# Kernel tuning notes

Hardware: AMD Instinct MI355X
Metric: run time of the kernel (lower is better)

Reference implementation:

```python
import jax, jax.numpy as jnp
import numpy as np

B, DIN, DOUT, GRID_SIZE, SPLINE_ORDER, N_LAYERS = 4096, 1024, 1024, 8, 3, 2
COEFFS = GRID_SIZE + SPLINE_ORDER  # 11


def _kaiming_uniform(key, shape, fan_in):
    # torch nn.init.kaiming_uniform_ default: a=0 -> gain=sqrt(2), bound=sqrt(3)*gain/sqrt(fan_in)
    bound = float(np.sqrt(6.0 / fan_in))
    return jax.random.uniform(key, shape, jnp.float32, -bound, bound)


def setup_inputs() -> dict:
    key = jax.random.key(0)
    ks = jax.random.split(key, 1 + 3 * N_LAYERS)
    x = jax.random.normal(ks[0], (B, DIN), dtype=jnp.float32)
    # knot grid: arange(-so, gs+so+1)*h + lo, h=(hi-lo)/gs  -> shape [GRID_SIZE+2*SPLINE_ORDER+1]
    h = 2.0 / GRID_SIZE
    grid = jnp.arange(-SPLINE_ORDER, GRID_SIZE + SPLINE_ORDER + 1, dtype=jnp.float32) * h - 1.0
    base_w, spline_w, scaler = [], [], []
    for i in range(N_LAYERS):
        base_w.append(_kaiming_uniform(ks[1 + 3 * i], (DOUT, DIN), DIN))
        spline_w.append(_kaiming_uniform(ks[2 + 3 * i], (DOUT, DIN, COEFFS), DIN * COEFFS))
        scaler.append(_kaiming_uniform(ks[3 + 3 * i], (DOUT, DIN), DIN))
    return {
        "x": x,
        "base_w": jnp.stack(base_w),      # [L, DOUT, DIN]
        "spline_w": jnp.stack(spline_w),  # [L, DOUT, DIN, COEFFS]
        "scaler": jnp.stack(scaler),      # [L, DOUT, DIN]
        "grid": grid,                      # [G]
        "spline_order": SPLINE_ORDER,
    }


def b_splines(x, grid, spline_order):
    # x: (B, DIN) -> bases: (B, DIN, COEFFS) via Cox-de Boor recursion
    x = x[..., None]  # (B, DIN, 1)
    bases = ((x >= grid[:-1]) & (x < grid[1:])).astype(x.dtype)  # order-0 indicators
    for k in range(1, spline_order + 1):
        left = (x - grid[: -(k + 1)]) / (grid[k:-1] - grid[: -(k + 1)])
        right = (grid[k + 1:] - x) / (grid[k + 1:] - grid[1:-k])
        bases = left * bases[..., :-1] + right * bases[..., 1:]
    return bases


def reference(x, base_w, spline_w, scaler, grid, spline_order):
    so = int(spline_order)
    n_layers = base_w.shape[0]
    for i in range(n_layers):
        x = jax.nn.silu(x)                                  # base_activation applied before both branches
        base_out = x @ base_w[i].T                          # (B, DOUT)
        bs = b_splines(x, grid, so)                         # (B, DIN, COEFFS)
        w = spline_w[i] * scaler[i][..., None]              # (DOUT, DIN, COEFFS)
        spline_out = jnp.einsum("bic,oic->bo", bs, w)      # == F.linear on flattened (DIN*COEFFS)
        x = base_out + spline_out
    return x
```

## Files before the change

kernel.cpp:

```cpp
#include <hip/hip_runtime.h>
#include <stdint.h>

#define BATCH 4096
#define DIN 1024
#define DOUT 1024
#define NC 11
#define KD 12288
#define NKNOTS 15

typedef __bf16 bf16x8 __attribute__((ext_vector_type(8)));
typedef float f32x4 __attribute__((ext_vector_type(4)));

__device__ __forceinline__ unsigned short f2bf(float f) {
    unsigned int u = __float_as_uint(f);
    unsigned int r = (u + 0x7FFFu + ((u >> 16) & 1u)) >> 16;
    return (unsigned short)r;
}

__global__ __launch_bounds__(256) void build_A(
    const float* __restrict__ x, const float* __restrict__ P, int np,
    const float* __restrict__ grid, unsigned short* __restrict__ A) {
    __shared__ __align__(16) unsigned short lbs[256 * NC];
    const int tid = threadIdx.x;
    const int b  = blockIdx.x >> 2;
    const int i0 = (blockIdx.x & 3) * 256;
    const int i  = i0 + tid;

    float g[NKNOTS];
#pragma unroll
    for (int j = 0; j < NKNOTS; ++j) g[j] = grid[j];

    float xv = x[(size_t)b * DIN + i];
    for (int p = 0; p < np; ++p)
        xv += P[(size_t)p * BATCH * DIN + (size_t)b * DIN + i];
    const float s = xv / (1.f + __expf(-xv));

    float bs[14];
#pragma unroll
    for (int c = 0; c < 14; ++c) bs[c] = (s >= g[c] && s < g[c + 1]) ? 1.f : 0.f;
#pragma unroll
    for (int k = 1; k <= 3; ++k) {
        const float inv = (k == 1) ? 4.f : (k == 2) ? 2.f : (4.f / 3.f);
#pragma unroll
        for (int c = 0; c < 14 - k; ++c) {
            float left  = (s - g[c]) * inv;
            float right = (g[c + k + 1] - s) * inv;
            bs[c] = left * bs[c] + right * bs[c + 1];
        }
    }

    A[(size_t)b * KD + i] = f2bf(s);
#pragma unroll
    for (int c = 0; c < NC; ++c) lbs[tid * NC + c] = f2bf(bs[c]);
    __syncthreads();

    const uint4* src = (const uint4*)lbs;
    uint4* dst = (uint4*)(A + (size_t)b * KD + DIN + (size_t)i0 * NC);
    for (int j = tid; j < 352; j += 256) dst[j] = src[j];
}

__global__ __launch_bounds__(256) void build_W(
    const float* __restrict__ base_w, const float* __restrict__ spline_w,
    const float* __restrict__ scaler, unsigned short* __restrict__ W) {
    __shared__ __align__(16) unsigned short lw[256 * NC];
    const int tid = threadIdx.x;
    const int o  = blockIdx.x >> 2;
    const int i0 = (blockIdx.x & 3) * 256;
    const int i  = i0 + tid;
    const size_t oi = (size_t)o * DIN + i;

    const float sc = scaler[oi];
    W[(size_t)o * KD + i] = f2bf(base_w[oi]);
    const float* sw = spline_w + oi * NC;
#pragma unroll
    for (int c = 0; c < NC; ++c) lw[tid * NC + c] = f2bf(sw[c] * sc);
    __syncthreads();

    const uint4* src = (const uint4*)lw;
    uint4* dst = (uint4*)(W + (size_t)o * KD + DIN + (size_t)i0 * NC);
    for (int j = tid; j < 352; j += 256) dst[j] = src[j];
}

#define BM 256
#define BN 256
#define BK 64

#define LOADAF(AF, BASE)                                                       \
    _Pragma("unroll")                                                          \
    for (int fm = 0; fm < 4; ++fm)                                             \
        _Pragma("unroll")                                                      \
        for (int ks = 0; ks < 2; ++ks)                                         \
            AF[fm][ks] = *(const bf16x8*)&(BASE)[(wm * 64 + fm * 16 + rof) * 64 + \
                                                 (((ks * 4 + kcol) ^ xr) * 8)];

#define LOADBF(BF, BASE)                                                       \
    _Pragma("unroll")                                                          \
    for (int fn = 0; fn < 2; ++fn)                                             \
        _Pragma("unroll")                                                      \
        for (int ks = 0; ks < 2; ++ks)                                         \
            BF[fn][ks] = *(const bf16x8*)&(BASE)[(wn * 32 + fn * 16 + rof) * 64 + \
                                                 (((ks * 4 + kcol) ^ xr) * 8)];

#define MFMA16(AF, BF, RO, CO)                                                 \
    __builtin_amdgcn_s_setprio(1);                                             \
    _Pragma("unroll")                                                          \
    for (int ks = 0; ks < 2; ++ks)                                             \
        _Pragma("unroll")                                                      \
        for (int fm = 0; fm < 4; ++fm)                                         \
            _Pragma("unroll")                                                  \
            for (int fn = 0; fn < 2; ++fn)                                     \
                acc[(RO) + fm][(CO) + fn] =                                    \
                    __builtin_amdgcn_mfma_f32_16x16x32_bf16(                   \
                        AF[fm][ks], BF[fn][ks], acc[(RO) + fm][(CO) + fn], 0, 0, 0); \
    __builtin_amdgcn_s_setprio(0);

#define SBAR  __builtin_amdgcn_s_barrier()
#define SCHED __builtin_amdgcn_sched_barrier(0)

__global__ __launch_bounds__(512, 2) void gemm_kan(
    const unsigned short* __restrict__ A,
    const unsigned short* __restrict__ W,
    float* __restrict__ C, float* __restrict__ Part,
    int kspl, int ktper) {
    __shared__ unsigned short As[2 * 2 * 8192];
    __shared__ unsigned short Bs[2 * 2 * 8192];

    const int tid  = threadIdx.x;
    const int wave = tid >> 6;
    const int lane = tid & 63;
    const int per = 16 * kspl;
    const int n0  = (blockIdx.x / per) * BN;
    const int r   = blockIdx.x % per;
    const int ksp = r % kspl;
    const int m0  = (r / kspl) * BM;
    const int wm = wave >> 2;
    const int wn = wave & 3;

    const int srow = lane >> 3;
    const int scol = 8 * ((lane & 7) ^ (lane >> 3));
    const int kbase = ksp * ktper * BK;

    f32x4 acc[8][4];
#pragma unroll
    for (int a = 0; a < 8; ++a)
#pragma unroll
        for (int b = 0; b < 4; ++b) acc[a][b] = (f32x4){0.f, 0.f, 0.f, 0.f};

    auto stageA = [&](int buf, int h, int kt) {
        const int kk = kbase + kt * BK + scol;
#pragma unroll
        for (int c = 0; c < 2; ++c) {
            const int chunk = wave * 2 + c;
            const unsigned short* ga =
                A + (size_t)(m0 + h * 128 + chunk * 8 + srow) * KD + kk;
            __builtin_amdgcn_global_load_lds(
                (const __attribute__((address_space(1))) unsigned int*)ga,
                (__attribute__((address_space(3))) unsigned int*)
                    &As[buf * 16384 + h * 8192 + chunk * 512], 16, 0, 0);
        }
    };
    auto stageB = [&](int buf, int h, int kt) {
        const int kk = kbase + kt * BK + scol;
#pragma unroll
        for (int c = 0; c < 2; ++c) {
            const int chunk = wave * 2 + c;
            const unsigned short* gb =
                W + (size_t)(n0 + h * 128 + chunk * 8 + srow) * KD + kk;
            __builtin_amdgcn_global_load_lds(
                (const __attribute__((address_space(1))) unsigned int*)gb,
                (__attribute__((address_space(3))) unsigned int*)
                    &Bs[buf * 16384 + h * 8192 + chunk * 512], 16, 0, 0);
        }
    };

    stageB(0, 0, 0); stageB(0, 1, 0); stageA(0, 0, 0); stageA(0, 1, 0);

    const int rof  = lane & 15;
    const int xr   = lane & 7;
    const int kcol = lane >> 4;

    for (int t = 0; t < ktper; ++t) {
        const int cur = t & 1;
        const int nxt = cur ^ 1;
        const unsigned short* Ab = &As[cur * 16384];
        const unsigned short* Bb = &Bs[cur * 16384];

        asm volatile("s_waitcnt vmcnt(0)" ::: "memory");
        SCHED;
        SBAR;
        SCHED;

        if (t + 1 < ktper) {
            stageB(nxt, 0, t + 1); stageB(nxt, 1, t + 1);
            stageA(nxt, 0, t + 1); stageA(nxt, 1, t + 1);
        }
        SCHED;

        bf16x8 a0[4][2], a1[4][2], b0[2][2], b1[2][2];
        LOADAF(a0, Ab);
        LOADBF(b0, Bb);
        LOADBF(b1, Bb + 8192);
        MFMA16(a0, b0, 0, 0);
        LOADAF(a1, Ab + 8192);
        MFMA16(a0, b1, 0, 2);
        MFMA16(a1, b1, 4, 2);
        MFMA16(a1, b0, 4, 0);
    }

    float* Cp = (ksp == 0) ? C : (Part + (size_t)(ksp - 1) * BATCH * DOUT);
    const int crow = (lane >> 4) * 4;
    const int ccol = lane & 15;
#pragma unroll
    for (int H = 0; H < 2; ++H)
#pragma unroll
        for (int fm = 0; fm < 4; ++fm)
#pragma unroll
            for (int F = 0; F < 2; ++F)
#pragma unroll
                for (int fn = 0; fn < 2; ++fn) {
                    const int row = m0 + H * 128 + wm * 64 + fm * 16 + crow;
                    const int col = n0 + F * 128 + wn * 32 + fn * 16 + ccol;
#pragma unroll
                    for (int rr = 0; rr < 4; ++rr)
                        Cp[(size_t)(row + rr) * DOUT + col] =
                            acc[H * 4 + fm][F * 2 + fn][rr];
                }
}

__global__ __launch_bounds__(256) void reduce_add(
    const float* __restrict__ P, float* __restrict__ X, int np) {
    const size_t i = ((size_t)blockIdx.x * 256 + threadIdx.x) * 4;
    f32x4 a = *(const f32x4*)(X + i);
    for (int p = 0; p < np; ++p)
        a = a + *(const f32x4*)(P + (size_t)p * BATCH * DOUT + i);
    *(f32x4*)(X + i) = a;
}

extern "C" void kernel_launch(void* const* d_in, const int* in_sizes, int n_in,
                              void* d_out, int out_size, void* d_ws, size_t ws_size,
                              hipStream_t stream) {
    const float* x        = (const float*)d_in[0];
    const float* base_w   = (const float*)d_in[1];
    const float* spline_w = (const float*)d_in[2];
    const float* scaler   = (const float*)d_in[3];
    const float* grid     = (const float*)d_in[4];
    float* out = (float*)d_out;

    char* ws = (char*)d_ws;
    unsigned short* Abf = (unsigned short*)ws;
    unsigned short* Wbf = (unsigned short*)(ws + 100663296);
    float* xtmp = (float*)(ws + 100663296 + 25165824);
    float* Part = (float*)(ws + 100663296 + 25165824 + 16777216);

    const size_t base_need = 100663296u + 25165824u + 16777216u;
    const int kspl = (ws_size >= base_need + 3u * 16777216u) ? 4 : 2;
    const int ktper = (KD / BK) / kspl;

    for (int layer = 0; layer < 2; ++layer) {
        const float* xin = (layer == 0) ? x : xtmp;
        float* xout      = (layer == 0) ? xtmp : out;
        build_W<<<4096, 256, 0, stream>>>(base_w + (size_t)layer * DOUT * DIN,
                                          spline_w + (size_t)layer * DOUT * DIN * NC,
                                          scaler + (size_t)layer * DOUT * DIN, Wbf);
        build_A<<<16384, 256, 0, stream>>>(xin, Part, (layer == 0) ? 0 : kspl - 1,
                                           grid, Abf);
        gemm_kan<<<64 * kspl, 512, 0, stream>>>(Abf, Wbf, xout, Part, kspl, ktper);
    }
    reduce_add<<<BATCH * DOUT / 1024, 256, 0, stream>>>(Part, out, kspl - 1);
}
```

Baseline: 306.8 us.

## Interleave quarter-tile prefetch with MFMA phases and partial vmcnt waits

Restructures the GEMM main loop so global-to-LDS staging of the next tile is split into quarter chunks issued between MFMA groups. Each chunk gets its own partial vmcnt wait and barrier, replacing the single full drain per iteration, and the next tile's first A/B fragments are preloaded at the end of the iteration. Part of A is staged two iterations ahead into the buffer being consumed. The aim is to hide load latency behind compute, at the cost of more barriers per iteration and fragile reliance on exact in-flight load counts.

```diff
diff --git a/kernel.cpp b/kernel.cpp
--- a/kernel.cpp
+++ b/kernel.cpp
@@ -173,38 +173,57 @@
         }
     };
 
-    stageB(0, 0, 0); stageB(0, 1, 0); stageA(0, 0, 0); stageA(0, 1, 0);
-
     const int rof  = lane & 15;
     const int xr   = lane & 7;
     const int kcol = lane >> 4;
 
+    bf16x8 a0[4][2], a1[4][2], b0[2][2], b1[2][2];
+
+    stageA(0, 0, 0); stageB(0, 0, 0); stageB(0, 1, 0); stageA(0, 1, 0);
+    if (ktper > 1) stageA(1, 0, 1);
+    if (ktper > 1) { asm volatile("s_waitcnt vmcnt(2)" ::: "memory"); }
+    else           { asm volatile("s_waitcnt vmcnt(0)" ::: "memory"); }
+    SBAR; SCHED;
+    LOADAF(a0, &As[0]);
+    LOADBF(b0, &Bs[0]);
+
     for (int t = 0; t < ktper; ++t) {
         const int cur = t & 1;
         const int nxt = cur ^ 1;
-        const unsigned short* Ab = &As[cur * 16384];
-        const unsigned short* Bb = &Bs[cur * 16384];
-
-        asm volatile("s_waitcnt vmcnt(0)" ::: "memory");
-        SCHED;
-        SBAR;
-        SCHED;
-
-        if (t + 1 < ktper) {
-            stageB(nxt, 0, t + 1); stageB(nxt, 1, t + 1);
-            stageA(nxt, 0, t + 1); stageA(nxt, 1, t + 1);
-        }
-        SCHED;
-
-        bf16x8 a0[4][2], a1[4][2], b0[2][2], b1[2][2];
-        LOADAF(a0, Ab);
-        LOADBF(b0, Bb);
+        const bool pf = (t + 1 < ktper);
+        const unsigned short* Ab  = &As[cur * 16384];
+        const unsigned short* Bb  = &Bs[cur * 16384];
+        const unsigned short* Abn = &As[nxt * 16384];
+        const unsigned short* Bbn = &Bs[nxt * 16384];
+
+        if (pf) stageB(nxt, 0, t + 1);
         LOADBF(b1, Bb + 8192);
         MFMA16(a0, b0, 0, 0);
+        SCHED;
+        if (pf) { asm volatile("s_waitcnt vmcnt(4)" ::: "memory"); }
+        else    { asm volatile("s_waitcnt vmcnt(0)" ::: "memory"); }
+        SBAR; SCHED;
+
+        if (pf) stageB(nxt, 1, t + 1);
         LOADAF(a1, Ab + 8192);
         MFMA16(a0, b1, 0, 2);
+        SCHED; SBAR; SCHED;
+
+        if (pf) stageA(nxt, 1, t + 1);
         MFMA16(a1, b1, 4, 2);
+        SCHED;
+        if (pf) { asm volatile("s_waitcnt vmcnt(4)" ::: "memory"); }
+        else    { asm volatile("s_waitcnt vmcnt(0)" ::: "memory"); }
+        SBAR; SCHED;
+
         MFMA16(a1, b0, 4, 0);
+        if (t + 2 < ktper) stageA(cur, 0, t + 2);
+        if (pf) { LOADAF(a0, Abn); LOADBF(b0, Bbn); }
+        SCHED;
+        if (t + 2 < ktper) { asm volatile("s_waitcnt vmcnt(4)" ::: "memory"); }
+        else if (pf)       { asm volatile("s_waitcnt vmcnt(2)" ::: "memory"); }
+        else               { asm volatile("s_waitcnt vmcnt(0)" ::: "memory"); }
+        SBAR; SCHED;
     }
 
     float* Cp = (ksp == 0) ? C : (Part + (size_t)(ksp - 1) * BATCH * DOUT);
```

Result: no change. 310.6 us (+1.3%).
